# Optimization experiments

Hardware: AMD Instinct MI355X
Metric: run time of the kernel (lower is better)

## Reference

```python
import jax, jax.numpy as jnp
import numpy as np

NEG_SLOPE = 0.2  # PyG GATv2Conv default leaky_relu slope


def _gatv2(x, src, dst, valid, Wl, bl, Wr, br, att, bias, concat):
    """Faithful PyG GATv2Conv (share_weights=False, add_self_loops=True).
    src/dst already include appended self loops; `valid` masks out original
    self-loop edges (remove_self_loops semantics) with fixed shapes.
    """
    N = x.shape[0]
    H, C = att.shape
    xl = (x @ Wl + bl).reshape(N, H, C)  # source transform
    xr = (x @ Wr + br).reshape(N, H, C)  # destination transform
    xj = xl[src]                          # [Etot,H,C] gathered messages
    e = jax.nn.leaky_relu(xr[dst] + xj, NEG_SLOPE)
    logits = jnp.einsum('ehc,hc->eh', e, att)  # [Etot,H]
    logits = jnp.where(valid[:, None], logits, -jnp.inf)
    # segment softmax over incoming edges of each dst node
    m = jax.ops.segment_max(logits, dst, num_segments=N)          # [N,H]
    m = jnp.where(jnp.isfinite(m), m, 0.0)
    ex = jnp.where(valid[:, None], jnp.exp(logits - m[dst]), 0.0)
    denom = jax.ops.segment_sum(ex, dst, num_segments=N)          # >0 (self loops)
    alpha = ex / denom[dst]                                       # [Etot,H]
    out = jax.ops.segment_sum(alpha[:, :, None] * xj, dst, num_segments=N)
    out = out.reshape(N, H * C) if concat else out.mean(axis=1)
    return out + bias


def _glorot(key, shape):
    fan = shape[0] + shape[-1] if len(shape) > 1 else shape[0]
    return jax.random.normal(key, shape, jnp.float32) * np.sqrt(2.0 / fan)


def setup_inputs() -> dict:
    key = jax.random.key(0)
    ks = jax.random.split(key, 24)
    N, E, F, B, NC = 50000, 800000, 32, 64, 10
    x = jax.random.normal(ks[0], (N, F), jnp.float32)
    edge_index = jax.random.randint(ks[1], (2, E), 0, N, jnp.int64)
    batch_index = jnp.sort(jax.random.randint(ks[2], (N,), 0, B, jnp.int64))
    d = {"x": x, "edge_index": edge_index, "batch_index": batch_index}
    # layer 0: 32 -> 64, heads=3, concat
    d["Wl0"] = _glorot(ks[3], (F, 192)); d["bl0"] = jnp.zeros((192,), jnp.float32)
    d["Wr0"] = _glorot(ks[4], (F, 192)); d["br0"] = jnp.zeros((192,), jnp.float32)
    d["att0"] = _glorot(ks[5], (3, 64)); d["bias0"] = jnp.zeros((192,), jnp.float32)
    # layer 1: 192 -> 64, heads=2, concat
    d["Wl1"] = _glorot(ks[6], (192, 128)); d["bl1"] = jnp.zeros((128,), jnp.float32)
    d["Wr1"] = _glorot(ks[7], (192, 128)); d["br1"] = jnp.zeros((128,), jnp.float32)
    d["att1"] = _glorot(ks[8], (2, 64)); d["bias1"] = jnp.zeros((128,), jnp.float32)
    # layer 2: 128 -> 64, heads=2, mean over heads
    d["Wl2"] = _glorot(ks[9], (128, 128)); d["bl2"] = jnp.zeros((128,), jnp.float32)
    d["Wr2"] = _glorot(ks[10], (128, 128)); d["br2"] = jnp.zeros((128,), jnp.float32)
    d["att2"] = _glorot(ks[11], (2, 64)); d["bias2"] = jnp.zeros((64,), jnp.float32)
    # output linear: 128 -> num_classes
    d["Wout"] = _glorot(ks[12], (128, NC)); d["bout"] = jnp.zeros((NC,), jnp.float32)
    return d


def reference(x, edge_index, batch_index,
              Wl0, bl0, Wr0, br0, att0, bias0,
              Wl1, bl1, Wr1, br1, att1, bias1,
              Wl2, bl2, Wr2, br2, att2, bias2,
              Wout, bout):
    N = x.shape[0]
    B = 64  # number of graphs
    loop = jnp.arange(N, dtype=edge_index.dtype)
    src = jnp.concatenate([edge_index[0], loop])
    dst = jnp.concatenate([edge_index[1], loop])
    valid = jnp.concatenate([edge_index[0] != edge_index[1],
                             jnp.ones((N,), bool)])  # drop accidental self loops

    h = jax.nn.relu(_gatv2(x, src, dst, valid, Wl0, bl0, Wr0, br0, att0, bias0, True))
    h = jax.nn.relu(_gatv2(h, src, dst, valid, Wl1, bl1, Wr1, br1, att1, bias1, True))
    h = jax.nn.relu(_gatv2(h, src, dst, valid, Wl2, bl2, Wr2, br2, att2, bias2, False))

    # global max pool + global mean pool over graphs
    gmx = jax.ops.segment_max(h, batch_index, num_segments=B)
    gmx = jnp.where(jnp.isfinite(gmx), gmx, 0.0)
    cnt = jax.ops.segment_sum(jnp.ones((N,), h.dtype), batch_index, num_segments=B)
    gmn = jax.ops.segment_sum(h, batch_index, num_segments=B) / jnp.maximum(cnt, 1.0)[:, None]
    pooled = jnp.concatenate([gmx, gmn], axis=1)  # [B, 128]
    return pooled @ Wout + bout
```

## Files before the change

### kernel.cpp

```cpp
#include <hip/hip_runtime.h>
#include <hip/hip_bf16.h>
#include <math.h>

#define NEG_SLOPE 0.2f

typedef __attribute__((ext_vector_type(8))) short short8;
typedef __attribute__((ext_vector_type(4))) float f32x4;

__device__ __forceinline__ unsigned short f2b(float v){
    unsigned int b = __float_as_uint(v);
    return (unsigned short)((b + 0x7FFFu + ((b >> 16) & 1u)) >> 16);
}

__device__ __forceinline__ float swz_add16(float p){
    int q;
    q = __builtin_amdgcn_ds_swizzle(__float_as_int(p), 0x041F); p += __int_as_float(q);
    q = __builtin_amdgcn_ds_swizzle(__float_as_int(p), 0x081F); p += __int_as_float(q);
    q = __builtin_amdgcn_ds_swizzle(__float_as_int(p), 0x101F); p += __int_as_float(q);
    q = __builtin_amdgcn_ds_swizzle(__float_as_int(p), 0x201F); p += __int_as_float(q);
    return p;
}


__global__ void edge_count(const int* __restrict__ src, const int* __restrict__ dst,
                           int E, int* __restrict__ counts){
    int e = blockIdx.x * blockDim.x + threadIdx.x;
    if (e >= E) return;
    int s = src[e], d = dst[e];
    if (s != d) atomicAdd(&counts[d], 1);
}

__global__ void scan_block(const int* __restrict__ counts, int* __restrict__ offsets,
                           int* __restrict__ blockSums, int N){
    __shared__ int sh[256];
    int t = threadIdx.x;
    int i = blockIdx.x * 256 + t;
    int v = (i < N) ? counts[i] : 0;
    sh[t] = v; __syncthreads();
    for (int off = 1; off < 256; off <<= 1){
        int x = (t >= off) ? sh[t - off] : 0;
        __syncthreads();
        sh[t] += x;
        __syncthreads();
    }
    if (i < N) offsets[i] = sh[t] - v;
    if (t == 255) blockSums[blockIdx.x] = sh[255];
}

__global__ void scan_sums(int* __restrict__ blockSums, int nb){
    __shared__ int sh[256];
    int t = threadIdx.x;
    int v = (t < nb) ? blockSums[t] : 0;
    sh[t] = v; __syncthreads();
    for (int off = 1; off < 256; off <<= 1){
        int x = (t >= off) ? sh[t - off] : 0;
        __syncthreads();
        sh[t] += x;
        __syncthreads();
    }
    if (t < nb) blockSums[t] = sh[t] - v;
}

__global__ void scan_add(int* __restrict__ offsets, const int* __restrict__ blockSums, int N){
    int i = blockIdx.x * 256 + threadIdx.x;
    if (i < N) offsets[i] += blockSums[blockIdx.x];
}

__global__ void copy_int(const int* __restrict__ a, int* __restrict__ b, int N){
    int i = blockIdx.x * blockDim.x + threadIdx.x;
    if (i < N) b[i] = a[i];
}

__global__ void edge_scatter(const int* __restrict__ src, const int* __restrict__ dst,
                             int E, int* __restrict__ cursor, int* __restrict__ edge_src){
    int e = blockIdx.x * blockDim.x + threadIdx.x;
    if (e >= E) return;
    int s = src[e], d = dst[e];
    if (s != d){
        int pos = atomicAdd(&cursor[d], 1);
        edge_src[pos] = s;
    }
}

__global__ void scale_edges(const int* __restrict__ es, int m,
                            int* __restrict__ e384, int* __restrict__ e256){
    int i = blockIdx.x * 256 + threadIdx.x;
    if (i >= m) return;
    int s = es[i];
    e384[i] = s * 384;
    e256[i] = s * 256;
}

__global__ void build_wt(const float* __restrict__ Wl, const float* __restrict__ Wr,
                         int K, int HC, unsigned short* __restrict__ WT, int total){
    int i = blockIdx.x * 256 + threadIdx.x;
    if (i >= total) return;
    int c = i / K, k = i - c * K;
    float v = (c < HC) ? Wl[(size_t)k * HC + c] : Wr[(size_t)k * HC + (c - HC)];
    WT[i] = f2b(v);
}

template<int K, int COLS, int HC, bool INB>
__global__ __launch_bounds__(256)
void mfma_dual_linear(const void* __restrict__ in_,
                      const unsigned short* __restrict__ WT,
                      const float* __restrict__ bl, const float* __restrict__ br,
                      unsigned short* __restrict__ xlb,
                      float* __restrict__ xr,
                      int N){
    constexpr int KP = K + 8;
    constexpr int CT = COLS / 64;
    __shared__ __align__(16) unsigned short xs[64 * KP];
    const int tid = threadIdx.x;
    const int row0 = blockIdx.x * 64;

    {
        const int r = tid >> 2, q = tid & 3;
        int gr = row0 + r; if (gr > N - 1) gr = N - 1;
        unsigned short* op = &xs[r * KP + q * (K / 4)];
        if (INB){
            const unsigned short* ip = (const unsigned short*)in_ + (size_t)gr * K + q * (K / 4);
            #pragma unroll
            for (int kk = 0; kk < K / 4; kk += 8)
                *(uint4*)&op[kk] = *(const uint4*)&ip[kk];
        } else {
            const float* ip = (const float*)in_ + (size_t)gr * K + q * (K / 4);
            #pragma unroll
            for (int kk = 0; kk < K / 4; kk += 4){
                float4 v = *(const float4*)&ip[kk];
                ushort4 o;
                o.x = f2b(v.x); o.y = f2b(v.y); o.z = f2b(v.z); o.w = f2b(v.w);
                *(ushort4*)&op[kk] = o;
            }
        }
    }
    __syncthreads();

    const int w = tid >> 6, lane = tid & 63;
    const int lr = lane & 15, lk = (lane >> 4) * 8;

    f32x4 acc[CT][4];
    #pragma unroll
    for (int ct = 0; ct < CT; ++ct){
        int c = (w * CT + ct) * 16 + lr;
        float bv = (c < HC) ? bl[c] : br[c - HC];
        #pragma unroll
        for (int rt = 0; rt < 4; ++rt) acc[ct][rt] = {bv, bv, bv, bv};
    }

    #pragma unroll
    for (int ks = 0; ks < K / 32; ++ks){
        short8 a[4];
        #pragma unroll
        for (int rt = 0; rt < 4; ++rt)
            a[rt] = *(const short8*)&xs[(rt * 16 + lr) * KP + ks * 32 + lk];
        #pragma unroll
        for (int ct = 0; ct < CT; ++ct){
            int c = (w * CT + ct) * 16 + lr;
            short8 b = *(const short8*)&WT[(size_t)c * K + ks * 32 + lk];
            #pragma unroll
            for (int rt = 0; rt < 4; ++rt)
                acc[ct][rt] = __builtin_amdgcn_mfma_f32_16x16x32_bf16(a[rt], b, acc[ct][rt], 0, 0, 0);
        }
    }

    #pragma unroll
    for (int ct = 0; ct < CT; ++ct){
        int c = (w * CT + ct) * 16 + lr;
        #pragma unroll
        for (int rt = 0; rt < 4; ++rt){
            #pragma unroll
            for (int r = 0; r < 4; ++r){
                int row = row0 + rt * 16 + (lane >> 4) * 4 + r;
                if (row < N){
                    float v = acc[ct][rt][r];
                    if (c < HC) xlb[(size_t)row * HC + c] = f2b(v);
                    else        xr [(size_t)row * HC + (c - HC)] = v;
                }
            }
        }
    }
}

template<int H, bool MEAN, bool OUTB>
__global__ __launch_bounds__(256)
void gatv2_agg(const unsigned short* __restrict__ xlb, const float* __restrict__ xr,
               const float* __restrict__ att, const float* __restrict__ bias,
               const int* __restrict__ offsets, const int* __restrict__ counts,
               const int* __restrict__ ebyte,
               void* __restrict__ hout, int N){
    const int HC = H * 64;
    const int RB = HC * 2;
    int wid  = (blockIdx.x * 256 + threadIdx.x) >> 6;
    int lane = threadIdx.x & 63;
    int g = lane >> 4, sl = lane & 15, cb = sl * 4;
    int n, h0, h1;
    if (MEAN){ n = wid; h0 = 0; h1 = H; }
    else     { n = wid / H; h0 = wid - n * H; h1 = h0 + 1; }
    if (n >= N) return;
    const int rs = offsets[n];
    const int total = counts[n] + 1;
    const char* XB = (const char*)xlb;
    const unsigned selfb = (unsigned)(n * RB);

    float ox = 0.f, oy = 0.f, oz = 0.f, ow = 0.f;
    for (int h = h0; h < h1; ++h){
        const float4 a4 = *(const float4*)&att[h * 64 + cb];
        const float4 q4 = *(const float4*)&xr[(size_t)n * HC + h * 64 + cb];
        const unsigned colb = (unsigned)((h * 64 + cb) * 2);
        float m = -INFINITY, den = 0.f;
        float ax = 0.f, ay = 0.f, az = 0.f, aw = 0.f;
        int vi = g;
        if (vi < total){
            unsigned boff = (g == 0) ? selfb : (unsigned)ebyte[rs + g - 1];
            uint2 u = *(const uint2*)(XB + (boff + colb));
            unsigned boffn = (unsigned)ebyte[rs + vi + 3];
            while (vi < total){
                int vin = vi + 4;
                uint2 un = *(const uint2*)(XB + (boffn + colb));
                boffn = (unsigned)ebyte[rs + vin + 3];
                float x0 = __uint_as_float(u.x << 16);
                float x1 = __uint_as_float(u.x & 0xFFFF0000u);
                float x2 = __uint_as_float(u.y << 16);
                float x3 = __uint_as_float(u.y & 0xFFFF0000u);
                float t0 = q4.x + x0, t1 = q4.y + x1;
                float t2 = q4.z + x2, t3 = q4.w + x3;
                t0 = fmaxf(t0, NEG_SLOPE * t0);
                t1 = fmaxf(t1, NEG_SLOPE * t1);
                t2 = fmaxf(t2, NEG_SLOPE * t2);
                t3 = fmaxf(t3, NEG_SLOPE * t3);
                float p = a4.x * t0 + a4.y * t1 + a4.z * t2 + a4.w * t3;
                p = swz_add16(p);
                float d = p - m;
                if (d > 8.f){
                    float s = __expf(-d);
                    den *= s; ax *= s; ay *= s; az *= s; aw *= s;
                    m = p; d = 0.f;
                }
                float eb = __expf(d);
                den += eb;
                ax += eb * x0; ay += eb * x1;
                az += eb * x2; aw += eb * x3;
                u = un; vi = vin;
            }
        }
        #pragma unroll
        for (int off = 16; off <= 32; off <<= 1){
            float mo  = __shfl_xor(m,  off, 64);
            float dno = __shfl_xor(den, off, 64);
            float bx = __shfl_xor(ax, off, 64), by = __shfl_xor(ay, off, 64);
            float bz = __shfl_xor(az, off, 64), bw = __shfl_xor(aw, off, 64);
            float Mn = fmaxf(m, mo);
            float sa = (m  == -INFINITY) ? 0.f : __expf(m  - Mn);
            float sb = (mo == -INFINITY) ? 0.f : __expf(mo - Mn);
            den = den * sa + dno * sb;
            ax = ax * sa + bx * sb; ay = ay * sa + by * sb;
            az = az * sa + bz * sb; aw = aw * sa + bw * sb;
            m = Mn;
        }
        float inv = 1.f / den;
        ox += ax * inv; oy += ay * inv; oz += az * inv; ow += aw * inv;
    }
    if (lane < 16){
        if (MEAN){
            const float s = 1.f / H;
            const float4 bv = *(const float4*)&bias[cb];
            float4 o;
            o.x = fmaxf(ox * s + bv.x, 0.f);
            o.y = fmaxf(oy * s + bv.y, 0.f);
            o.z = fmaxf(oz * s + bv.z, 0.f);
            o.w = fmaxf(ow * s + bv.w, 0.f);
            *(float4*)&((float*)hout)[(size_t)n * 64 + cb] = o;
        } else {
            const float4 bv = *(const float4*)&bias[h0 * 64 + cb];
            float o0 = fmaxf(ox + bv.x, 0.f), o1 = fmaxf(oy + bv.y, 0.f);
            float o2 = fmaxf(oz + bv.z, 0.f), o3 = fmaxf(ow + bv.w, 0.f);
            if (OUTB){
                uint2 w2;
                w2.x = (unsigned)f2b(o0) | ((unsigned)f2b(o1) << 16);
                w2.y = (unsigned)f2b(o2) | ((unsigned)f2b(o3) << 16);
                *(uint2*)&((unsigned short*)hout)[(size_t)n * HC + h0 * 64 + cb] = w2;
            } else {
                float4 o; o.x = o0; o.y = o1; o.z = o2; o.w = o3;
                *(float4*)&((float*)hout)[(size_t)n * HC + h0 * 64 + cb] = o;
            }
        }
    }
}

__global__ __launch_bounds__(256)
void pool_kernel(const float* __restrict__ h, const int* __restrict__ batch,
                 int N, float* __restrict__ gmx, float* __restrict__ gsum,
                 int* __restrict__ gcnt){
    const int lane = threadIdx.x & 63;
    const int w = threadIdx.x >> 6;
    const int n0 = blockIdx.x * 256;
    const int nend = min(n0 + 256, N);
    float rmax = 0.f, rsum = 0.f;
    int curG = -1, cnt = 0;
    for (int n = n0 + w; n < nend; n += 4){
        int g = batch[n];
        float v = h[(size_t)n * 64 + lane];
        if (g != curG){
            if (curG >= 0){
                atomicMax((int*)&gmx[curG * 64 + lane], __float_as_int(rmax));
                atomicAdd(&gsum[curG * 64 + lane], rsum);
                if (lane == 0) atomicAdd(&gcnt[curG], cnt);
            }
            curG = g; rmax = v; rsum = v; cnt = 1;
        } else {
            rmax = fmaxf(rmax, v); rsum += v; ++cnt;
        }
    }
    if (curG >= 0){
        atomicMax((int*)&gmx[curG * 64 + lane], __float_as_int(rmax));
        atomicAdd(&gsum[curG * 64 + lane], rsum);
        if (lane == 0) atomicAdd(&gcnt[curG], cnt);
    }
}

__global__ void final_linear(const float* __restrict__ gmx, const float* __restrict__ gsum,
                             const int* __restrict__ gcnt,
                             const float* __restrict__ Wout, const float* __restrict__ bout,
                             float* __restrict__ out){
    int t = threadIdx.x;
    if (t >= 640) return;
    int g = t / 10, oc = t % 10;
    float cnt = (float)max(gcnt[g], 1);
    float acc = bout[oc];
    for (int k = 0; k < 64; ++k)  acc += gmx[g * 64 + k] * Wout[k * 10 + oc];
    for (int k = 0; k < 64; ++k)  acc += (gsum[g * 64 + k] / cnt) * Wout[(64 + k) * 10 + oc];
    out[g * 10 + oc] = acc;
}

extern "C" void kernel_launch(void* const* d_in, const int* in_sizes, int n_in,
                              void* d_out, int out_size, void* d_ws, size_t ws_size,
                              hipStream_t stream){
    const int N = 50000, E = 800000, B = 64;
    const float* x    = (const float*)d_in[0];
    const int*  ei    = (const int*)d_in[1];
    const int*  batch = (const int*)d_in[2];
    const float *Wl0=(const float*)d_in[3],  *bl0=(const float*)d_in[4],
                *Wr0=(const float*)d_in[5],  *br0=(const float*)d_in[6],
                *att0=(const float*)d_in[7], *bias0=(const float*)d_in[8];
    const float *Wl1=(const float*)d_in[9],  *bl1=(const float*)d_in[10],
                *Wr1=(const float*)d_in[11], *br1=(const float*)d_in[12],
                *att1=(const float*)d_in[13],*bias1=(const float*)d_in[14];
    const float *Wl2=(const float*)d_in[15], *bl2=(const float*)d_in[16],
                *Wr2=(const float*)d_in[17], *br2=(const float*)d_in[18],
                *att2=(const float*)d_in[19],*bias2=(const float*)d_in[20];
    const float *Wout=(const float*)d_in[21],*bout=(const float*)d_in[22];

    const int* srcA = ei;
    const int* dstA = ei + E;

    char* p = (char*)d_ws;
    auto alloc = [&](size_t bytes)->void*{ void* r = (void*)p; p += (bytes + 255) & ~(size_t)255; return r; };
    void*  bufA   = alloc((size_t)N * 192 * 4);
    float* bufC   = (float*)alloc((size_t)N * 192 * 4);
    unsigned short* xlb = (unsigned short*)alloc((size_t)N * 192 * 2);
    unsigned short* WT0 = (unsigned short*)alloc((size_t)384 * 32 * 2);
    unsigned short* WT1 = (unsigned short*)alloc((size_t)256 * 192 * 2);
    unsigned short* WT2 = (unsigned short*)alloc((size_t)256 * 128 * 2);
    int* counts   = (int*)alloc((size_t)N * 4);
    int* offsets  = (int*)alloc((size_t)N * 4);
    int* cursor   = (int*)alloc((size_t)N * 4);
    int* blockSums= (int*)alloc(256 * 4);
    int* edge_src = (int*)alloc((size_t)(E + 8) * 4);
    int* eb384    = (int*)alloc((size_t)(E + 8) * 4);
    int* eb256    = (int*)alloc((size_t)(E + 8) * 4);
    float* gmx    = (float*)alloc((size_t)B * 64 * 4);
    float* gsum   = (float*)alloc((size_t)B * 64 * 4);
    int* gcnt     = (int*)alloc((size_t)B * 4);

    build_wt<<<(384 * 32 + 255) / 256, 256, 0, stream>>>(Wl0, Wr0, 32, 192, WT0, 384 * 32);
    build_wt<<<(256 * 192 + 255) / 256, 256, 0, stream>>>(Wl1, Wr1, 192, 128, WT1, 256 * 192);
    build_wt<<<(256 * 128 + 255) / 256, 256, 0, stream>>>(Wl2, Wr2, 128, 128, WT2, 256 * 128);

    hipMemsetAsync(counts, 0, (size_t)N * 4, stream);
    hipMemsetAsync(edge_src, 0, (size_t)(E + 8) * 4, stream);
    int eb = (E + 255) / 256;
    int nb = (N + 255) / 256;
    edge_count<<<eb, 256, 0, stream>>>(srcA, dstA, E, counts);
    scan_block<<<nb, 256, 0, stream>>>(counts, offsets, blockSums, N);
    scan_sums<<<1, 256, 0, stream>>>(blockSums, nb);
    scan_add<<<nb, 256, 0, stream>>>(offsets, blockSums, N);
    copy_int<<<nb, 256, 0, stream>>>(offsets, cursor, N);
    edge_scatter<<<eb, 256, 0, stream>>>(srcA, dstA, E, cursor, edge_src);
    scale_edges<<<(E + 8 + 255) / 256, 256, 0, stream>>>(edge_src, E + 8, eb384, eb256);

    const int rb = (N + 63) / 64;

    mfma_dual_linear<32, 384, 192, false><<<rb, 256, 0, stream>>>(x, WT0, bl0, br0, xlb, bufC, N);
    gatv2_agg<3, false, true><<<(N * 3 + 3) / 4, 256, 0, stream>>>(xlb, bufC, att0, bias0, offsets, counts, eb384, bufA, N);

    mfma_dual_linear<192, 256, 128, true><<<rb, 256, 0, stream>>>(bufA, WT1, bl1, br1, xlb, bufC, N);
    gatv2_agg<2, false, true><<<(N * 2 + 3) / 4, 256, 0, stream>>>(xlb, bufC, att1, bias1, offsets, counts, eb256, bufA, N);

    mfma_dual_linear<128, 256, 128, true><<<rb, 256, 0, stream>>>(bufA, WT2, bl2, br2, xlb, bufC, N);
    gatv2_agg<2, true, false><<<(N + 3) / 4, 256, 0, stream>>>(xlb, bufC, att2, bias2, offsets, counts, eb256, bufA, N);

    hipMemsetAsync(gmx,  0, (size_t)B * 64 * 4, stream);
    hipMemsetAsync(gsum, 0, (size_t)B * 64 * 4, stream);
    hipMemsetAsync(gcnt, 0, (size_t)B * 4, stream);
    pool_kernel<<<(N + 255) / 256, 256, 0, stream>>>((const float*)bufA, batch, N, gmx, gsum, gcnt);
    final_linear<<<1, 640, 0, stream>>>(gmx, gsum, gcnt, Wout, bout, (float*)d_out);
}
```

Baseline: 409.7 us.

## Widen aggregation to 8 edges per wave, use packed FP32 math, fuse setup kernels

The GATv2 aggregation kernel now assigns 8 lanes per edge with 8 channels each, so a wave processes 8 edges at once using 16-byte loads. It also moves the per-edge arithmetic to packed v_pk FP32 instructions and shortens the cross-lane reduction. The setup stage merges the three weight-transpose launches into one, folds the offset copy into the scan and the edge scaling into the scatter, and zeroes the pooling buffers with a single memset. final_linear now stages its inputs in shared memory. The wider edge batching holds more registers per lane and reads further ahead in the edge list, which is why the edge arrays get more padding.

```diff
diff --git a/kernel.cpp b/kernel.cpp
--- a/kernel.cpp
+++ b/kernel.cpp
@@ -6,18 +6,35 @@
 
 typedef __attribute__((ext_vector_type(8))) short short8;
 typedef __attribute__((ext_vector_type(4))) float f32x4;
+typedef __attribute__((ext_vector_type(2))) float f32x2;
 
 __device__ __forceinline__ unsigned short f2b(float v){
     unsigned int b = __float_as_uint(v);
     return (unsigned short)((b + 0x7FFFu + ((b >> 16) & 1u)) >> 16);
 }
 
-__device__ __forceinline__ float swz_add16(float p){
+__device__ __forceinline__ f32x2 pk_add(f32x2 a, f32x2 b){
+    f32x2 d; asm("v_pk_add_f32 %0, %1, %2" : "=v"(d) : "v"(a), "v"(b)); return d;
+}
+__device__ __forceinline__ f32x2 pk_mul(f32x2 a, f32x2 b){
+    f32x2 d; asm("v_pk_mul_f32 %0, %1, %2" : "=v"(d) : "v"(a), "v"(b)); return d;
+}
+__device__ __forceinline__ f32x2 pk_fma(f32x2 a, f32x2 b, f32x2 c){
+    f32x2 d; asm("v_pk_fma_f32 %0, %1, %2, %3" : "=v"(d) : "v"(a), "v"(b), "v"(c)); return d;
+}
+
+__device__ __forceinline__ f32x2 unpk(unsigned v){
+    f32x2 r;
+    r.x = __uint_as_float(v << 16);
+    r.y = __uint_as_float(v & 0xFFFF0000u);
+    return r;
+}
+
+__device__ __forceinline__ float swz_add8(float p){
     int q;
     q = __builtin_amdgcn_ds_swizzle(__float_as_int(p), 0x041F); p += __int_as_float(q);
     q = __builtin_amdgcn_ds_swizzle(__float_as_int(p), 0x081F); p += __int_as_float(q);
     q = __builtin_amdgcn_ds_swizzle(__float_as_int(p), 0x101F); p += __int_as_float(q);
-    q = __builtin_amdgcn_ds_swizzle(__float_as_int(p), 0x201F); p += __int_as_float(q);
     return p;
 }
 
@@ -61,43 +78,51 @@
     if (t < nb) blockSums[t] = sh[t] - v;
 }
 
-__global__ void scan_add(int* __restrict__ offsets, const int* __restrict__ blockSums, int N){
+__global__ void scan_add(int* __restrict__ offsets, int* __restrict__ cursor,
+                         const int* __restrict__ blockSums, int N){
     int i = blockIdx.x * 256 + threadIdx.x;
-    if (i < N) offsets[i] += blockSums[blockIdx.x];
-}
-
-__global__ void copy_int(const int* __restrict__ a, int* __restrict__ b, int N){
-    int i = blockIdx.x * blockDim.x + threadIdx.x;
-    if (i < N) b[i] = a[i];
+    if (i < N){
+        int v = offsets[i] + blockSums[blockIdx.x];
+        offsets[i] = v;
+        cursor[i]  = v;
+    }
 }
 
 __global__ void edge_scatter(const int* __restrict__ src, const int* __restrict__ dst,
-                             int E, int* __restrict__ cursor, int* __restrict__ edge_src){
+                             int E, int* __restrict__ cursor,
+                             int* __restrict__ e384, int* __restrict__ e256){
     int e = blockIdx.x * blockDim.x + threadIdx.x;
     if (e >= E) return;
     int s = src[e], d = dst[e];
     if (s != d){
         int pos = atomicAdd(&cursor[d], 1);
-        edge_src[pos] = s;
-    }
-}
-
-__global__ void scale_edges(const int* __restrict__ es, int m,
-                            int* __restrict__ e384, int* __restrict__ e256){
+        e384[pos] = s * 384;
+        e256[pos] = s * 256;
+    }
+}
+
+__global__ void build_wt_all(const float* __restrict__ Wl0, const float* __restrict__ Wr0,
+                             const float* __restrict__ Wl1, const float* __restrict__ Wr1,
+                             const float* __restrict__ Wl2, const float* __restrict__ Wr2,
+                             unsigned short* __restrict__ WT0,
+                             unsigned short* __restrict__ WT1,
+                             unsigned short* __restrict__ WT2){
     int i = blockIdx.x * 256 + threadIdx.x;
-    if (i >= m) return;
-    int s = es[i];
-    e384[i] = s * 384;
-    e256[i] = s * 256;
-}
-
-__global__ void build_wt(const float* __restrict__ Wl, const float* __restrict__ Wr,
-                         int K, int HC, unsigned short* __restrict__ WT, int total){
-    int i = blockIdx.x * 256 + threadIdx.x;
-    if (i >= total) return;
-    int c = i / K, k = i - c * K;
-    float v = (c < HC) ? Wl[(size_t)k * HC + c] : Wr[(size_t)k * HC + (c - HC)];
-    WT[i] = f2b(v);
+    if (i < 12288){
+        int c = i / 32, k = i - c * 32;
+        float v = (c < 192) ? Wl0[(size_t)k * 192 + c] : Wr0[(size_t)k * 192 + (c - 192)];
+        WT0[i] = f2b(v);
+    } else if (i < 61440){
+        int j = i - 12288;
+        int c = j / 192, k = j - c * 192;
+        float v = (c < 128) ? Wl1[(size_t)k * 128 + c] : Wr1[(size_t)k * 128 + (c - 128)];
+        WT1[j] = f2b(v);
+    } else if (i < 94208){
+        int j = i - 61440;
+        int c = j / 128, k = j - c * 128;
+        float v = (c < 128) ? Wl2[(size_t)k * 128 + c] : Wr2[(size_t)k * 128 + (c - 128)];
+        WT2[j] = f2b(v);
+    }
 }
 
 template<int K, int COLS, int HC, bool INB>
@@ -193,7 +218,7 @@
     const int RB = HC * 2;
     int wid  = (blockIdx.x * 256 + threadIdx.x) >> 6;
     int lane = threadIdx.x & 63;
-    int g = lane >> 4, sl = lane & 15, cb = sl * 4;
+    int g = lane >> 3, sl = lane & 7, cb = sl * 8;
     int n, h0, h1;
     if (MEAN){ n = wid; h0 = 0; h1 = H; }
     else     { n = wid / H; h0 = wid - n * H; h1 = h0 + 1; }
@@ -202,88 +227,112 @@
     const int total = counts[n] + 1;
     const char* XB = (const char*)xlb;
     const unsigned selfb = (unsigned)(n * RB);
-
-    float ox = 0.f, oy = 0.f, oz = 0.f, ow = 0.f;
+    const f32x2 ns2 = {NEG_SLOPE, NEG_SLOPE};
+
+    f32x2 o2[4] = {{0.f,0.f},{0.f,0.f},{0.f,0.f},{0.f,0.f}};
     for (int h = h0; h < h1; ++h){
-        const float4 a4 = *(const float4*)&att[h * 64 + cb];
-        const float4 q4 = *(const float4*)&xr[(size_t)n * HC + h * 64 + cb];
+        const float4 aa = *(const float4*)&att[h * 64 + cb];
+        const float4 ab = *(const float4*)&att[h * 64 + cb + 4];
+        const float4 qa = *(const float4*)&xr[(size_t)n * HC + h * 64 + cb];
+        const float4 qb = *(const float4*)&xr[(size_t)n * HC + h * 64 + cb + 4];
+        const f32x2 q2[4] = {{qa.x,qa.y},{qa.z,qa.w},{qb.x,qb.y},{qb.z,qb.w}};
+        const f32x2 a2[4] = {{aa.x,aa.y},{aa.z,aa.w},{ab.x,ab.y},{ab.z,ab.w}};
         const unsigned colb = (unsigned)((h * 64 + cb) * 2);
         float m = -INFINITY, den = 0.f;
-        float ax = 0.f, ay = 0.f, az = 0.f, aw = 0.f;
+        f32x2 acc2[4] = {{0.f,0.f},{0.f,0.f},{0.f,0.f},{0.f,0.f}};
         int vi = g;
         if (vi < total){
             unsigned boff = (g == 0) ? selfb : (unsigned)ebyte[rs + g - 1];
-            uint2 u = *(const uint2*)(XB + (boff + colb));
-            unsigned boffn = (unsigned)ebyte[rs + vi + 3];
+            uint4 u = *(const uint4*)(XB + (boff + colb));
+            unsigned boffn = (unsigned)ebyte[rs + vi + 7];
             while (vi < total){
-                int vin = vi + 4;
-                uint2 un = *(const uint2*)(XB + (boffn + colb));
-                boffn = (unsigned)ebyte[rs + vin + 3];
-                float x0 = __uint_as_float(u.x << 16);
-                float x1 = __uint_as_float(u.x & 0xFFFF0000u);
-                float x2 = __uint_as_float(u.y << 16);
-                float x3 = __uint_as_float(u.y & 0xFFFF0000u);
-                float t0 = q4.x + x0, t1 = q4.y + x1;
-                float t2 = q4.z + x2, t3 = q4.w + x3;
-                t0 = fmaxf(t0, NEG_SLOPE * t0);
-                t1 = fmaxf(t1, NEG_SLOPE * t1);
-                t2 = fmaxf(t2, NEG_SLOPE * t2);
-                t3 = fmaxf(t3, NEG_SLOPE * t3);
-                float p = a4.x * t0 + a4.y * t1 + a4.z * t2 + a4.w * t3;
-                p = swz_add16(p);
+                int vin = vi + 8;
+                uint4 un = *(const uint4*)(XB + (boffn + colb));
+                boffn = (unsigned)ebyte[rs + vin + 7];
+                f32x2 x0 = unpk(u.x), x1 = unpk(u.y), x2 = unpk(u.z), x3 = unpk(u.w);
+                f32x2 t0 = pk_add(q2[0], x0), t1 = pk_add(q2[1], x1);
+                f32x2 t2 = pk_add(q2[2], x2), t3 = pk_add(q2[3], x3);
+                f32x2 s0 = pk_mul(t0, ns2), s1 = pk_mul(t1, ns2);
+                f32x2 s2 = pk_mul(t2, ns2), s3 = pk_mul(t3, ns2);
+                t0.x = fmaxf(t0.x, s0.x); t0.y = fmaxf(t0.y, s0.y);
+                t1.x = fmaxf(t1.x, s1.x); t1.y = fmaxf(t1.y, s1.y);
+                t2.x = fmaxf(t2.x, s2.x); t2.y = fmaxf(t2.y, s2.y);
+                t3.x = fmaxf(t3.x, s3.x); t3.y = fmaxf(t3.y, s3.y);
+                f32x2 dp0 = pk_mul(a2[0], t0);
+                f32x2 dp1 = pk_mul(a2[1], t1);
+                dp0 = pk_fma(a2[2], t2, dp0);
+                dp1 = pk_fma(a2[3], t3, dp1);
+                dp0 = pk_add(dp0, dp1);
+                float p = dp0.x + dp0.y;
+                p = swz_add8(p);
                 float d = p - m;
                 if (d > 8.f){
                     float s = __expf(-d);
-                    den *= s; ax *= s; ay *= s; az *= s; aw *= s;
+                    f32x2 sv = {s, s};
+                    den *= s;
+                    acc2[0] = pk_mul(acc2[0], sv); acc2[1] = pk_mul(acc2[1], sv);
+                    acc2[2] = pk_mul(acc2[2], sv); acc2[3] = pk_mul(acc2[3], sv);
                     m = p; d = 0.f;
                 }
                 float eb = __expf(d);
                 den += eb;
-                ax += eb * x0; ay += eb * x1;
-                az += eb * x2; aw += eb * x3;
+                f32x2 e2 = {eb, eb};
+                acc2[0] = pk_fma(e2, x0, acc2[0]); acc2[1] = pk_fma(e2, x1, acc2[1]);
+                acc2[2] = pk_fma(e2, x2, acc2[2]); acc2[3] = pk_fma(e2, x3, acc2[3]);
                 u = un; vi = vin;
             }
         }
         #pragma unroll
-        for (int off = 16; off <= 32; off <<= 1){
+        for (int off = 8; off <= 32; off <<= 1){
             float mo  = __shfl_xor(m,  off, 64);
             float dno = __shfl_xor(den, off, 64);
-            float bx = __shfl_xor(ax, off, 64), by = __shfl_xor(ay, off, 64);
-            float bz = __shfl_xor(az, off, 64), bw = __shfl_xor(aw, off, 64);
+            f32x2 b0, b1, b2, b3;
+            b0.x = __shfl_xor(acc2[0].x, off, 64); b0.y = __shfl_xor(acc2[0].y, off, 64);
+            b1.x = __shfl_xor(acc2[1].x, off, 64); b1.y = __shfl_xor(acc2[1].y, off, 64);
+            b2.x = __shfl_xor(acc2[2].x, off, 64); b2.y = __shfl_xor(acc2[2].y, off, 64);
+            b3.x = __shfl_xor(acc2[3].x, off, 64); b3.y = __shfl_xor(acc2[3].y, off, 64);
             float Mn = fmaxf(m, mo);
             float sa = (m  == -INFINITY) ? 0.f : __expf(m  - Mn);
             float sb = (mo == -INFINITY) ? 0.f : __expf(mo - Mn);
             den = den * sa + dno * sb;
-            ax = ax * sa + bx * sb; ay = ay * sa + by * sb;
-            az = az * sa + bz * sb; aw = aw * sa + bw * sb;
+            f32x2 sa2 = {sa, sa}, sb2 = {sb, sb};
+            acc2[0] = pk_fma(acc2[0], sa2, pk_mul(b0, sb2));
+            acc2[1] = pk_fma(acc2[1], sa2, pk_mul(b1, sb2));
+            acc2[2] = pk_fma(acc2[2], sa2, pk_mul(b2, sb2));
+            acc2[3] = pk_fma(acc2[3], sa2, pk_mul(b3, sb2));
             m = Mn;
         }
         float inv = 1.f / den;
-        ox += ax * inv; oy += ay * inv; oz += az * inv; ow += aw * inv;
-    }
-    if (lane < 16){
+        f32x2 i2 = {inv, inv};
         if (MEAN){
-            const float s = 1.f / H;
-            const float4 bv = *(const float4*)&bias[cb];
-            float4 o;
-            o.x = fmaxf(ox * s + bv.x, 0.f);
-            o.y = fmaxf(oy * s + bv.y, 0.f);
-            o.z = fmaxf(oz * s + bv.z, 0.f);
-            o.w = fmaxf(ow * s + bv.w, 0.f);
-            *(float4*)&((float*)hout)[(size_t)n * 64 + cb] = o;
+            o2[0] = pk_fma(acc2[0], i2, o2[0]); o2[1] = pk_fma(acc2[1], i2, o2[1]);
+            o2[2] = pk_fma(acc2[2], i2, o2[2]); o2[3] = pk_fma(acc2[3], i2, o2[3]);
         } else {
-            const float4 bv = *(const float4*)&bias[h0 * 64 + cb];
-            float o0 = fmaxf(ox + bv.x, 0.f), o1 = fmaxf(oy + bv.y, 0.f);
-            float o2 = fmaxf(oz + bv.z, 0.f), o3 = fmaxf(ow + bv.w, 0.f);
-            if (OUTB){
-                uint2 w2;
-                w2.x = (unsigned)f2b(o0) | ((unsigned)f2b(o1) << 16);
-                w2.y = (unsigned)f2b(o2) | ((unsigned)f2b(o3) << 16);
-                *(uint2*)&((unsigned short*)hout)[(size_t)n * HC + h0 * 64 + cb] = w2;
-            } else {
-                float4 o; o.x = o0; o.y = o1; o.z = o2; o.w = o3;
-                *(float4*)&((float*)hout)[(size_t)n * HC + h0 * 64 + cb] = o;
-            }
+            o2[0] = pk_mul(acc2[0], i2); o2[1] = pk_mul(acc2[1], i2);
+            o2[2] = pk_mul(acc2[2], i2); o2[3] = pk_mul(acc2[3], i2);
+        }
+    }
+    if (lane < 8){
+        const int bb0 = (MEAN ? 0 : h0 * 64) + cb;
+        const float4 ba = *(const float4*)&bias[bb0];
+        const float4 bbv = *(const float4*)&bias[bb0 + 4];
+        const float sc = MEAN ? (1.f / H) : 1.f;
+        float r0 = fmaxf(o2[0].x * sc + ba.x,  0.f), r1 = fmaxf(o2[0].y * sc + ba.y,  0.f);
+        float r2 = fmaxf(o2[1].x * sc + ba.z,  0.f), r3 = fmaxf(o2[1].y * sc + ba.w,  0.f);
+        float r4 = fmaxf(o2[2].x * sc + bbv.x, 0.f), r5 = fmaxf(o2[2].y * sc + bbv.y, 0.f);
+        float r6 = fmaxf(o2[3].x * sc + bbv.z, 0.f), r7 = fmaxf(o2[3].y * sc + bbv.w, 0.f);
+        if (OUTB){
+            uint4 w4;
+            w4.x = (unsigned)f2b(r0) | ((unsigned)f2b(r1) << 16);
+            w4.y = (unsigned)f2b(r2) | ((unsigned)f2b(r3) << 16);
+            w4.z = (unsigned)f2b(r4) | ((unsigned)f2b(r5) << 16);
+            w4.w = (unsigned)f2b(r6) | ((unsigned)f2b(r7) << 16);
+            *(uint4*)&((unsigned short*)hout)[(size_t)n * HC + h0 * 64 + cb] = w4;
+        } else {
+            const size_t base = (size_t)n * (MEAN ? 64 : HC) + (MEAN ? 0 : h0 * 64) + cb;
+            float4 wa = {r0, r1, r2, r3}, wb = {r4, r5, r6, r7};
+            *(float4*)&((float*)hout)[base]     = wa;
+            *(float4*)&((float*)hout)[base + 4] = wb;
         }
     }
 }
@@ -319,18 +368,23 @@
     }
 }
 
-__global__ void final_linear(const float* __restrict__ gmx, const float* __restrict__ gsum,
-                             const int* __restrict__ gcnt,
-                             const float* __restrict__ Wout, const float* __restrict__ bout,
-                             float* __restrict__ out){
+__global__ __launch_bounds__(640)
+void final_linear(const float* __restrict__ gmx, const float* __restrict__ gsum,
+                  const int* __restrict__ gcnt,
+                  const float* __restrict__ Wout, const float* __restrict__ bout,
+                  float* __restrict__ out){
+    __shared__ float sg[4096], ss[4096];
     int t = threadIdx.x;
-    if (t >= 640) return;
+    for (int i = t; i < 4096; i += 640){ sg[i] = gmx[i]; ss[i] = gsum[i]; }
+    __syncthreads();
     int g = t / 10, oc = t % 10;
-    float cnt = (float)max(gcnt[g], 1);
-    float acc = bout[oc];
-    for (int k = 0; k < 64; ++k)  acc += gmx[g * 64 + k] * Wout[k * 10 + oc];
-    for (int k = 0; k < 64; ++k)  acc += (gsum[g * 64 + k] / cnt) * Wout[(64 + k) * 10 + oc];
-    out[g * 10 + oc] = acc;
+    float icnt = 1.f / (float)max(gcnt[g], 1);
+    float acc = bout[oc], accs = 0.f;
+    #pragma unroll 4
+    for (int k = 0; k < 64; ++k) acc  += sg[g * 64 + k] * Wout[k * 10 + oc];
+    #pragma unroll 4
+    for (int k = 0; k < 64; ++k) accs += ss[g * 64 + k] * Wout[(64 + k) * 10 + oc];
+    out[g * 10 + oc] = acc + accs * icnt;
 }
 
 extern "C" void kernel_launch(void* const* d_in, const int* in_sizes, int n_in,
@@ -366,28 +420,25 @@
     int* offsets  = (int*)alloc((size_t)N * 4);
     int* cursor   = (int*)alloc((size_t)N * 4);
     int* blockSums= (int*)alloc(256 * 4);
-    int* edge_src = (int*)alloc((size_t)(E + 8) * 4);
-    int* eb384    = (int*)alloc((size_t)(E + 8) * 4);
-    int* eb256    = (int*)alloc((size_t)(E + 8) * 4);
-    float* gmx    = (float*)alloc((size_t)B * 64 * 4);
-    float* gsum   = (float*)alloc((size_t)B * 64 * 4);
-    int* gcnt     = (int*)alloc((size_t)B * 4);
-
-    build_wt<<<(384 * 32 + 255) / 256, 256, 0, stream>>>(Wl0, Wr0, 32, 192, WT0, 384 * 32);
-    build_wt<<<(256 * 192 + 255) / 256, 256, 0, stream>>>(Wl1, Wr1, 192, 128, WT1, 256 * 192);
-    build_wt<<<(256 * 128 + 255) / 256, 256, 0, stream>>>(Wl2, Wr2, 128, 128, WT2, 256 * 128);
+    int* eb384    = (int*)alloc((size_t)(E + 24) * 4);
+    int* eb256    = (int*)alloc((size_t)(E + 24) * 4);
+    float* pool   = (float*)alloc((size_t)(B * 128 + B) * 4);
+    float* gmx  = pool;
+    float* gsum = pool + B * 64;
+    int*   gcnt = (int*)(pool + B * 128);
+
+    build_wt_all<<<(94208 + 255) / 256, 256, 0, stream>>>(Wl0, Wr0, Wl1, Wr1, Wl2, Wr2, WT0, WT1, WT2);
 
     hipMemsetAsync(counts, 0, (size_t)N * 4, stream);
-    hipMemsetAsync(edge_src, 0, (size_t)(E + 8) * 4, stream);
+    hipMemsetAsync(eb384, 0, (size_t)(E + 24) * 4, stream);
+    hipMemsetAsync(eb256, 0, (size_t)(E + 24) * 4, stream);
     int eb = (E + 255) / 256;
     int nb = (N + 255) / 256;
     edge_count<<<eb, 256, 0, stream>>>(srcA, dstA, E, counts);
     scan_block<<<nb, 256, 0, stream>>>(counts, offsets, blockSums, N);
     scan_sums<<<1, 256, 0, stream>>>(blockSums, nb);
-    scan_add<<<nb, 256, 0, stream>>>(offsets, blockSums, N);
-    copy_int<<<nb, 256, 0, stream>>>(offsets, cursor, N);
-    edge_scatter<<<eb, 256, 0, stream>>>(srcA, dstA, E, cursor, edge_src);
-    scale_edges<<<(E + 8 + 255) / 256, 256, 0, stream>>>(edge_src, E + 8, eb384, eb256);
+    scan_add<<<nb, 256, 0, stream>>>(offsets, cursor, blockSums, N);
+    edge_scatter<<<eb, 256, 0, stream>>>(srcA, dstA, E, cursor, eb384, eb256);
 
     const int rb = (N + 63) / 64;
 
@@ -400,9 +451,7 @@
     mfma_dual_linear<128, 256, 128, true><<<rb, 256, 0, stream>>>(bufA, WT2, bl2, br2, xlb, bufC, N);
     gatv2_agg<2, true, false><<<(N + 3) / 4, 256, 0, stream>>>(xlb, bufC, att2, bias2, offsets, counts, eb256, bufA, N);
 
-    hipMemsetAsync(gmx,  0, (size_t)B * 64 * 4, stream);
-    hipMemsetAsync(gsum, 0, (size_t)B * 64 * 4, stream);
-    hipMemsetAsync(gcnt, 0, (size_t)B * 4, stream);
+    hipMemsetAsync(pool, 0, (size_t)(B * 128 + B) * 4, stream);
     pool_kernel<<<(N + 255) / 256, 256, 0, stream>>>((const float*)bufA, batch, N, gmx, gsum, gcnt);
     final_linear<<<1, 640, 0, stream>>>(gmx, gsum, gcnt, Wout, bout, (float*)d_out);
 }
```

After: 438.6 us. 1.07x slower.
